# Kernel optimization log

Measured on AMD Instinct MI355X. Metric: run time of the kernel, lower is better.

The kernel has to match this reference:

```python
import jax, jax.numpy as jnp
import numpy as np

N, B, D_STREAM = 2048, 2, 1024
HEADS, D_KQ, D_V = 16, 64, 64
D_HEAD = 2 * D_KQ + D_V  # per-head [q|k|v] chunk


def setup_inputs() -> dict:
    key = jax.random.key(0)
    ks = jax.random.split(key, 6)
    s = 0.02
    return {
        "stream": jax.random.normal(ks[0], (N, B, D_STREAM), jnp.float32),
        "mask": jax.random.normal(ks[1], (1, N, N), jnp.float32),
        "w_qkv": jax.random.normal(ks[2], (D_STREAM, HEADS * D_HEAD), jnp.float32) * s,
        "b_qkv": jax.random.normal(ks[3], (HEADS * D_HEAD,), jnp.float32) * s,
        "w_out": jax.random.normal(ks[4], (HEADS * D_V, D_STREAM), jnp.float32) * s,
        "b_out": jax.random.normal(ks[5], (D_STREAM,), jnp.float32) * s,
    }


def reference(stream, mask, w_qkv, b_qkv, w_out, b_out):
    n, b, _ = stream.shape
    # qkv: (n, b, heads*(2*d_kq+d_v)) -> (n, b*heads, 2*d_kq+d_v)
    qkv = (stream @ w_qkv + b_qkv).reshape(n, b * HEADS, D_HEAD)
    q = qkv[:, :, :D_KQ]              # (n, bh, d_kq)
    k = qkv[:, :, D_KQ:2 * D_KQ]      # (n, bh, d_kq)
    v = qkv[:, :, 2 * D_KQ:]          # (n, bh, d_v)
    # logits: (bh, n, n); NOTE: no 1/sqrt(d_kq) scaling, faithful to source
    logits = jnp.einsum("nhd,mhd->hnm", q, k) + mask
    weights = jax.nn.softmax(logits, axis=-1)
    values = jnp.einsum("hnm,mhd->nhd", weights, v)  # (n, bh, d_v)
    values = values.reshape(n * b, HEADS * D_V)
    out = (values @ w_out + b_out).reshape(n, b, D_STREAM)
    return out
```

## Files before the change

kernel.cpp:

```cpp
#include <hip/hip_runtime.h>
#include <hip/hip_bf16.h>

#define N_SEQ 2048
#define DSTR 1024
#define NH 32
#define QKVN 3072
#define MROWS 4096

typedef float f32x4 __attribute__((ext_vector_type(4)));
typedef short bf16x8 __attribute__((ext_vector_type(8)));
typedef unsigned short ushort4v __attribute__((ext_vector_type(4)));
typedef unsigned short u16t;

__device__ __forceinline__ u16t f2bf(float f) {
  union { float f; unsigned u; } x; x.f = f;
  return (u16t)((x.u + 0x7fff + ((x.u >> 16) & 1)) >> 16);
}
__device__ __forceinline__ float bf2f(u16t u) {
  union { unsigned u; float f; } x; x.u = ((unsigned)u) << 16; return x.f;
}
__device__ __forceinline__ unsigned cvt_pk_bf16(float a, float b) {
  unsigned r;
  asm("v_cvt_pk_bf16_f32 %0, %1, %2" : "=v"(r) : "v"(a), "v"(b));
  return r;
}

#define MFMA16(a, b, c) __builtin_amdgcn_mfma_f32_16x16x32_bf16(a, b, c, 0, 0, 0)

__device__ __forceinline__ void gl2lds16(const void* g, void* l) {
  __builtin_amdgcn_global_load_lds((const __attribute__((address_space(1))) void*)g,
                                   (__attribute__((address_space(3))) void*)l, 16, 0, 0);
}

__global__ void split_f32_kernel(const float* __restrict__ in, u16t* __restrict__ hi,
                                 u16t* __restrict__ lo, int n4) {
  int i = blockIdx.x * blockDim.x + threadIdx.x;
  if (i >= n4) return;
  float4 v = ((const float4*)in)[i];
  float vv[4] = {v.x, v.y, v.z, v.w};
  ushort4v h, l;
  #pragma unroll
  for (int j = 0; j < 4; j++) {
    h[j] = f2bf(vv[j]);
    l[j] = f2bf(vv[j] - bf2f(h[j]));
  }
  ((ushort4v*)hi)[i] = h;
  if (lo) ((ushort4v*)lo)[i] = l;
}

__global__ void transpose_split_kernel(const float* __restrict__ in,
                                       u16t* __restrict__ hi, u16t* __restrict__ lo,
                                       int K, int Nc) {
  __shared__ float tile[32][33];
  const int n0 = blockIdx.x * 32, k0 = blockIdx.y * 32;
  const int tx = threadIdx.x, ty = threadIdx.y;
  #pragma unroll
  for (int j = 0; j < 32; j += 8)
    tile[ty + j][tx] = in[(size_t)(k0 + ty + j) * Nc + n0 + tx];
  __syncthreads();
  #pragma unroll
  for (int j = 0; j < 32; j += 8) {
    float v = tile[tx][ty + j];
    size_t o = (size_t)(n0 + ty + j) * K + k0 + tx;
    u16t h = f2bf(v);
    hi[o] = h;
    if (lo) lo[o] = f2bf(v - bf2f(h));
  }
}

__global__ __launch_bounds__(256, 3) void gemm_qkv_kernel(
    const u16t* __restrict__ Ahi, const u16t* __restrict__ Alo,
    const u16t* __restrict__ Bhi, const float* __restrict__ bias,
    u16t* __restrict__ Qhi, u16t* __restrict__ Qlo,
    u16t* __restrict__ Khi, u16t* __restrict__ Vt) {
  constexpr int BK = 64;
  __shared__ u16t sAh[128 * 64], sAl[128 * 64], sBh[128 * 64];
  const int t = threadIdx.x;
  const int lane = t & 63, wid = t >> 6;
  const int wm = wid >> 1, wn = wid & 1;
  const int g = lane >> 4, cc = lane & 15;
  const int m0 = blockIdx.x * 128, n0 = blockIdx.y * 128;
  const int srow = t >> 3;
  const int sc = ((t & 7) ^ ((t >> 3) & 7)) * 8;

  f32x4 acc[4][4] = {};

  for (int k0 = 0; k0 < DSTR; k0 += BK) {
    __syncthreads();
    #pragma unroll
    for (int i = 0; i < 4; i++) {
      const int row = i * 32 + srow;
      gl2lds16(Ahi + (size_t)(m0 + row) * DSTR + k0 + sc, &sAh[i * 2048 + wid * 512]);
      gl2lds16(Alo + (size_t)(m0 + row) * DSTR + k0 + sc, &sAl[i * 2048 + wid * 512]);
      gl2lds16(Bhi + (size_t)(n0 + row) * DSTR + k0 + sc, &sBh[i * 2048 + wid * 512]);
    }
    __syncthreads();
    #pragma unroll
    for (int kk = 0; kk < 2; kk++) {
      bf16x8 ah[4], al[4], bh[4];
      #pragma unroll
      for (int mt = 0; mt < 4; mt++) {
        const int r = wm * 64 + mt * 16 + cc;
        const int c = ((4 * kk + g) ^ (cc & 7)) * 8;
        ah[mt] = *(const bf16x8*)&sAh[r * 64 + c];
        al[mt] = *(const bf16x8*)&sAl[r * 64 + c];
      }
      #pragma unroll
      for (int nt = 0; nt < 4; nt++) {
        const int r = wn * 64 + nt * 16 + cc;
        const int c = ((4 * kk + g) ^ (cc & 7)) * 8;
        bh[nt] = *(const bf16x8*)&sBh[r * 64 + c];
      }
      #pragma unroll
      for (int mt = 0; mt < 4; mt++)
        #pragma unroll
        for (int nt = 0; nt < 4; nt++) {
          acc[mt][nt] = MFMA16(ah[mt], bh[nt], acc[mt][nt]);
          acc[mt][nt] = MFMA16(al[mt], bh[nt], acc[mt][nt]);
        }
    }
  }
  #pragma unroll
  for (int mt = 0; mt < 4; mt++)
    #pragma unroll
    for (int nt = 0; nt < 4; nt++)
      #pragma unroll
      for (int r = 0; r < 4; r++) {
        int grow = m0 + wm * 64 + mt * 16 + g * 4 + r;
        int gcol = n0 + wn * 64 + nt * 16 + cc;
        float val = acc[mt][nt][r] + bias[gcol];
        int nn = grow >> 1, bb = grow & 1;
        int hl = gcol / 192, off = gcol - hl * 192;
        int hh = bb * 16 + hl;
        if (off < 64) {
          size_t o = ((size_t)hh * N_SEQ + nn) * 64 + off;
          u16t h_ = f2bf(val);
          Qhi[o] = h_;
          Qlo[o] = f2bf(val - bf2f(h_));
        } else if (off < 128) {
          Khi[((size_t)hh * N_SEQ + nn) * 64 + (off - 64)] = f2bf(val);
        } else {
          int c = nn & 63;
          int nperm = (nn & ~63) | ((c & 15) << 2) | (c >> 4);
          Vt[((size_t)hh * 64 + (off - 128)) * N_SEQ + nperm] = f2bf(val);
        }
      }
}

__global__ __launch_bounds__(512, 4) void attn_kernel(
    const u16t* __restrict__ Qhi, const u16t* __restrict__ Qlo,
    const u16t* __restrict__ Khi, const u16t* __restrict__ Vt,
    const u16t* __restrict__ maskT, u16t* __restrict__ Vals) {
  __shared__ u16t sKh[2][64 * 64];
  __shared__ u16t sV[2][64 * 64];
  __shared__ u16t sP[8][16 * 72];
  const int t = threadIdx.x;
  const int lane = t & 63, wid = t >> 6;
  const int g = lane >> 4, cc = lane & 15;
  const int h = blockIdx.x >> 4;
  const int qt = blockIdx.x & 15;
  const int q0 = qt * 128 + wid * 16;

  const size_t kbase = (size_t)h * N_SEQ * 64;
  const size_t vbase = (size_t)h * 64 * N_SEQ;

  const int srow = t >> 3;
  const int ssw = ((t & 7) ^ (srow & 7)) * 8;
  const int wbase = wid * 512;

  auto stage = [&](int buf, int mt0) {
    gl2lds16(Khi + kbase + (size_t)(mt0 + srow) * 64 + ssw, &sKh[buf][wbase]);
    gl2lds16(Vt + vbase + (size_t)srow * N_SEQ + mt0 + ssw, &sV[buf][wbase]);
  };

  const size_t qoff = kbase + (size_t)(q0 + cc) * 64 + g * 8;
  bf16x8 qh0 = *(const bf16x8*)(Qhi + qoff);
  bf16x8 qh1 = *(const bf16x8*)(Qhi + qoff + 32);
  bf16x8 ql0 = *(const bf16x8*)(Qlo + qoff);
  bf16x8 ql1 = *(const bf16x8*)(Qlo + qoff + 32);

  f32x4 o[4] = {};
  float M[4], L[4];
  #pragma unroll
  for (int r = 0; r < 4; r++) { M[r] = -1e30f; L[r] = 0.0f; }

  stage(0, 0);
  int cur = 0;
  const int sw = (cc & 7) * 8;

  for (int ti = 0; ti < N_SEQ / 64; ++ti) {
    const int mt0 = ti * 64;
    __syncthreads();
    if (ti + 1 < N_SEQ / 64) stage(cur ^ 1, mt0 + 64);

    ushort4v ml[4];
    #pragma unroll
    for (int mt = 0; mt < 4; ++mt)
      ml[mt] = *(const ushort4v*)&maskT[(size_t)(mt0 + mt * 16 + cc) * N_SEQ + q0 + g * 4];

    f32x4 s[4];
    #pragma unroll
    for (int mt = 0; mt < 4; ++mt) {
      const int krow = (mt * 16 + cc) * 64;
      bf16x8 kh0 = *(const bf16x8*)&sKh[cur][krow + ((g * 8) ^ sw)];
      bf16x8 kh1 = *(const bf16x8*)&sKh[cur][krow + ((32 + g * 8) ^ sw)];
      f32x4 a = {};
      a = MFMA16(qh0, kh0, a);
      a = MFMA16(qh1, kh1, a);
      a = MFMA16(ql0, kh0, a);
      a = MFMA16(ql1, kh1, a);
      s[mt] = a;
    }
    float mx[4];
    #pragma unroll
    for (int r = 0; r < 4; ++r) {
      s[0][r] += bf2f(ml[0][r]);
      s[1][r] += bf2f(ml[1][r]);
      s[2][r] += bf2f(ml[2][r]);
      s[3][r] += bf2f(ml[3][r]);
      float m1 = fmaxf(fmaxf(s[0][r], s[1][r]), fmaxf(s[2][r], s[3][r]));
      m1 = fmaxf(m1, __shfl_xor(m1, 1, 16));
      m1 = fmaxf(m1, __shfl_xor(m1, 2, 16));
      m1 = fmaxf(m1, __shfl_xor(m1, 4, 16));
      m1 = fmaxf(m1, __shfl_xor(m1, 8, 16));
      mx[r] = m1;
    }
    float dm = fmaxf(fmaxf(mx[0] - M[0], mx[1] - M[1]),
                     fmaxf(mx[2] - M[2], mx[3] - M[3]));
    if (__any(dm > 8.0f)) {
      #pragma unroll
      for (int r = 0; r < 4; ++r) {
        float nM = fmaxf(M[r], mx[r]);
        float al = __expf(M[r] - nM);
        L[r] *= al;
        o[0][r] *= al; o[1][r] *= al; o[2][r] *= al; o[3][r] *= al;
        M[r] = nM;
      }
    }
    #pragma unroll
    for (int r = 0; r < 4; ++r) {
      float p0 = __expf(s[0][r] - M[r]);
      float p1 = __expf(s[1][r] - M[r]);
      float p2 = __expf(s[2][r] - M[r]);
      float p3 = __expf(s[3][r] - M[r]);
      float rs = (p0 + p1) + (p2 + p3);
      rs += __shfl_xor(rs, 1, 16);
      rs += __shfl_xor(rs, 2, 16);
      rs += __shfl_xor(rs, 4, 16);
      rs += __shfl_xor(rs, 8, 16);
      L[r] += rs;
      unsigned w0 = cvt_pk_bf16(p0, p1);
      unsigned w1 = cvt_pk_bf16(p2, p3);
      u16t* P = &sP[wid][(g * 4 + r) * 72 + cc * 4];
      P[0] = (u16t)w0; P[1] = (u16t)(w0 >> 16);
      P[2] = (u16t)w1; P[3] = (u16t)(w1 >> 16);
    }
    bf16x8 pf0 = *(const bf16x8*)&sP[wid][cc * 72 + g * 8];
    bf16x8 pf1 = *(const bf16x8*)&sP[wid][cc * 72 + 32 + g * 8];
    #pragma unroll
    for (int dt = 0; dt < 4; ++dt) {
      const int vrow = (dt * 16 + cc) * 64;
      bf16x8 v0 = *(const bf16x8*)&sV[cur][vrow + ((g * 8) ^ sw)];
      bf16x8 v1 = *(const bf16x8*)&sV[cur][vrow + ((32 + g * 8) ^ sw)];
      o[dt] = MFMA16(pf0, v0, o[dt]);
      o[dt] = MFMA16(pf1, v1, o[dt]);
    }
    cur ^= 1;
  }
  const int bb = h >> 4, hl = h & 15;
  #pragma unroll
  for (int r = 0; r < 4; ++r) {
    const int q = q0 + g * 4 + r;
    float invL = 1.0f / L[r];
    const size_t orow = (size_t)(q * 2 + bb) * DSTR + hl * 64;
    #pragma unroll
    for (int dt = 0; dt < 4; ++dt)
      Vals[orow + dt * 16 + cc] = f2bf(o[dt][r] * invL);
  }
}

__global__ __launch_bounds__(256, 3) void gemm_out_kernel(
    const u16t* __restrict__ A, const u16t* __restrict__ Bt,
    const float* __restrict__ bias, float* __restrict__ out) {
  constexpr int BK = 64;
  __shared__ u16t sA[128 * 64], sB[128 * 64];
  const int t = threadIdx.x;
  const int lane = t & 63, wid = t >> 6;
  const int wm = wid >> 1, wn = wid & 1;
  const int g = lane >> 4, cc = lane & 15;
  const int m0 = blockIdx.x * 128, n0 = blockIdx.y * 128;
  const int srow = t >> 3;
  const int sc = ((t & 7) ^ ((t >> 3) & 7)) * 8;

  f32x4 acc[4][4] = {};
  for (int k0 = 0; k0 < DSTR; k0 += BK) {
    __syncthreads();
    #pragma unroll
    for (int i = 0; i < 4; i++) {
      const int row = i * 32 + srow;
      gl2lds16(A + (size_t)(m0 + row) * DSTR + k0 + sc, &sA[i * 2048 + wid * 512]);
      gl2lds16(Bt + (size_t)(n0 + row) * DSTR + k0 + sc, &sB[i * 2048 + wid * 512]);
    }
    __syncthreads();
    #pragma unroll
    for (int kk = 0; kk < 2; kk++) {
      bf16x8 af[4], bfr[4];
      #pragma unroll
      for (int mt = 0; mt < 4; mt++) {
        const int r = wm * 64 + mt * 16 + cc;
        const int c = ((4 * kk + g) ^ (cc & 7)) * 8;
        af[mt] = *(const bf16x8*)&sA[r * 64 + c];
      }
      #pragma unroll
      for (int nt = 0; nt < 4; nt++) {
        const int r = wn * 64 + nt * 16 + cc;
        const int c = ((4 * kk + g) ^ (cc & 7)) * 8;
        bfr[nt] = *(const bf16x8*)&sB[r * 64 + c];
      }
      #pragma unroll
      for (int mt = 0; mt < 4; mt++)
        #pragma unroll
        for (int nt = 0; nt < 4; nt++)
          acc[mt][nt] = MFMA16(af[mt], bfr[nt], acc[mt][nt]);
    }
  }
  #pragma unroll
  for (int mt = 0; mt < 4; mt++)
    #pragma unroll
    for (int nt = 0; nt < 4; nt++)
      #pragma unroll
      for (int r = 0; r < 4; r++) {
        int grow = m0 + wm * 64 + mt * 16 + g * 4 + r;
        int gcol = n0 + wn * 64 + nt * 16 + cc;
        out[(size_t)grow * DSTR + gcol] = acc[mt][nt][r] + bias[gcol];
      }
}

extern "C" void kernel_launch(void* const* d_in, const int* in_sizes, int n_in,
                              void* d_out, int out_size, void* d_ws, size_t ws_size,
                              hipStream_t stream) {
  (void)in_sizes; (void)n_in; (void)out_size; (void)ws_size;
  const float* x      = (const float*)d_in[0];
  const float* mask   = (const float*)d_in[1];
  const float* w_qkv  = (const float*)d_in[2];
  const float* b_qkv  = (const float*)d_in[3];
  const float* w_out  = (const float*)d_in[4];
  const float* b_out  = (const float*)d_in[5];
  float* out = (float*)d_out;

  char* ws = (char*)d_ws;
  size_t off = 0;
  auto alloc = [&](size_t n) { void* p = ws + off; off += (n + 255) & ~(size_t)255; return p; };
  u16t* WqkvT = (u16t*)alloc((size_t)QKVN * DSTR * 2);
  u16t* WoutT = (u16t*)alloc((size_t)DSTR * DSTR * 2);
  u16t* Qhi = (u16t*)alloc((size_t)NH * N_SEQ * 64 * 2);
  u16t* Qlo = (u16t*)alloc((size_t)NH * N_SEQ * 64 * 2);
  u16t* Khi = (u16t*)alloc((size_t)NH * N_SEQ * 64 * 2);
  u16t* Vt  = (u16t*)alloc((size_t)NH * 64 * N_SEQ * 2);
  u16t* Xhi = (u16t*)alloc((size_t)MROWS * DSTR * 2);
  u16t* Xlo = (u16t*)alloc((size_t)MROWS * DSTR * 2);
  u16t* MaskT = (u16t*)alloc((size_t)N_SEQ * N_SEQ * 2);
  u16t* Vals = Xhi;

  split_f32_kernel<<<dim3(MROWS * DSTR / 4 / 256), 256, 0, stream>>>(x, Xhi, Xlo, MROWS * DSTR / 4);
  transpose_split_kernel<<<dim3(QKVN / 32, DSTR / 32), dim3(32, 8), 0, stream>>>(
      w_qkv, WqkvT, nullptr, DSTR, QKVN);
  transpose_split_kernel<<<dim3(DSTR / 32, DSTR / 32), dim3(32, 8), 0, stream>>>(
      w_out, WoutT, nullptr, DSTR, DSTR);
  transpose_split_kernel<<<dim3(N_SEQ / 32, N_SEQ / 32), dim3(32, 8), 0, stream>>>(
      mask, MaskT, nullptr, N_SEQ, N_SEQ);
  gemm_qkv_kernel<<<dim3(MROWS / 128, QKVN / 128), 256, 0, stream>>>(
      Xhi, Xlo, WqkvT, b_qkv, Qhi, Qlo, Khi, Vt);
  attn_kernel<<<dim3(NH * (N_SEQ / 128)), 512, 0, stream>>>(
      Qhi, Qlo, Khi, Vt, MaskT, Vals);
  gemm_out_kernel<<<dim3(MROWS / 128, DSTR / 128), 256, 0, stream>>>(
      Vals, WoutT, b_out, out);
}
```

Before: 272.8 us.

## Compute transposed scores in attention, fold log2e into Q and mask, shrink blocks

The QK MFMA operands are swapped so each lane holds scores for a single query row. Row max and sum then need only two cross-lane shuffles, with one M and L per lane instead of four. The log2e factor is folded into Q in the QKV epilogue and into the mask during conversion, so the softmax can use a raw v_exp_f32; the mask no longer needs a transpose pass and the V permutation is dropped. Attention blocks shrink from 512 to 256 threads over 64 queries, which doubles the grid. The P tile now uses an XOR-swizzled layout, and the rescale threshold becomes a base-2 equivalent.

```diff
diff --git a/kernel.cpp b/kernel.cpp
--- a/kernel.cpp
+++ b/kernel.cpp
@@ -6,6 +6,7 @@
 #define NH 32
 #define QKVN 3072
 #define MROWS 4096
+#define LOG2E 1.4426950408889634f
 
 typedef float f32x4 __attribute__((ext_vector_type(4)));
 typedef short bf16x8 __attribute__((ext_vector_type(8)));
@@ -24,6 +25,11 @@
   asm("v_cvt_pk_bf16_f32 %0, %1, %2" : "=v"(r) : "v"(a), "v"(b));
   return r;
 }
+__device__ __forceinline__ float exp2a(float x) {
+  float r;
+  asm("v_exp_f32 %0, %1" : "=v"(r) : "v"(x));
+  return r;
+}
 
 #define MFMA16(a, b, c) __builtin_amdgcn_mfma_f32_16x16x32_bf16(a, b, c, 0, 0, 0)
 
@@ -33,11 +39,11 @@
 }
 
 __global__ void split_f32_kernel(const float* __restrict__ in, u16t* __restrict__ hi,
-                                 u16t* __restrict__ lo, int n4) {
+                                 u16t* __restrict__ lo, int n4, float scale) {
   int i = blockIdx.x * blockDim.x + threadIdx.x;
   if (i >= n4) return;
   float4 v = ((const float4*)in)[i];
-  float vv[4] = {v.x, v.y, v.z, v.w};
+  float vv[4] = {v.x * scale, v.y * scale, v.z * scale, v.w * scale};
   ushort4v h, l;
   #pragma unroll
   for (int j = 0; j < 4; j++) {
@@ -133,6 +139,7 @@
         int hl = gcol / 192, off = gcol - hl * 192;
         int hh = bb * 16 + hl;
         if (off < 64) {
+          val *= LOG2E;
           size_t o = ((size_t)hh * N_SEQ + nn) * 64 + off;
           u16t h_ = f2bf(val);
           Qhi[o] = h_;
@@ -140,37 +147,36 @@
         } else if (off < 128) {
           Khi[((size_t)hh * N_SEQ + nn) * 64 + (off - 64)] = f2bf(val);
         } else {
-          int c = nn & 63;
-          int nperm = (nn & ~63) | ((c & 15) << 2) | (c >> 4);
-          Vt[((size_t)hh * 64 + (off - 128)) * N_SEQ + nperm] = f2bf(val);
+          Vt[((size_t)hh * 64 + (off - 128)) * N_SEQ + nn] = f2bf(val);
         }
       }
 }
 
-__global__ __launch_bounds__(512, 4) void attn_kernel(
+__global__ __launch_bounds__(256, 4) void attn_kernel(
     const u16t* __restrict__ Qhi, const u16t* __restrict__ Qlo,
     const u16t* __restrict__ Khi, const u16t* __restrict__ Vt,
-    const u16t* __restrict__ maskT, u16t* __restrict__ Vals) {
+    const u16t* __restrict__ maskb, u16t* __restrict__ Vals) {
   __shared__ u16t sKh[2][64 * 64];
   __shared__ u16t sV[2][64 * 64];
-  __shared__ u16t sP[8][16 * 72];
+  __shared__ u16t sP[4][16 * 64];
   const int t = threadIdx.x;
   const int lane = t & 63, wid = t >> 6;
   const int g = lane >> 4, cc = lane & 15;
-  const int h = blockIdx.x >> 4;
-  const int qt = blockIdx.x & 15;
-  const int q0 = qt * 128 + wid * 16;
+  const int h = blockIdx.x >> 5;
+  const int qt = blockIdx.x & 31;
+  const int q0 = qt * 64 + wid * 16;
 
   const size_t kbase = (size_t)h * N_SEQ * 64;
   const size_t vbase = (size_t)h * 64 * N_SEQ;
 
   const int srow = t >> 3;
-  const int ssw = ((t & 7) ^ (srow & 7)) * 8;
-  const int wbase = wid * 512;
+  const int sc = ((t & 7) ^ ((t >> 3) & 7)) * 8;
 
   auto stage = [&](int buf, int mt0) {
-    gl2lds16(Khi + kbase + (size_t)(mt0 + srow) * 64 + ssw, &sKh[buf][wbase]);
-    gl2lds16(Vt + vbase + (size_t)srow * N_SEQ + mt0 + ssw, &sV[buf][wbase]);
+    gl2lds16(Khi + kbase + (size_t)(mt0 + srow) * 64 + sc,      &sKh[buf][wid * 512]);
+    gl2lds16(Khi + kbase + (size_t)(mt0 + srow + 32) * 64 + sc, &sKh[buf][2048 + wid * 512]);
+    gl2lds16(Vt + vbase + (size_t)srow * N_SEQ + mt0 + sc,        &sV[buf][wid * 512]);
+    gl2lds16(Vt + vbase + (size_t)(srow + 32) * N_SEQ + mt0 + sc, &sV[buf][2048 + wid * 512]);
   };
 
   const size_t qoff = kbase + (size_t)(q0 + cc) * 64 + g * 8;
@@ -180,13 +186,13 @@
   bf16x8 ql1 = *(const bf16x8*)(Qlo + qoff + 32);
 
   f32x4 o[4] = {};
-  float M[4], L[4];
-  #pragma unroll
-  for (int r = 0; r < 4; r++) { M[r] = -1e30f; L[r] = 0.0f; }
+  float M = -1e30f, L = 0.0f;
 
   stage(0, 0);
   int cur = 0;
   const int sw = (cc & 7) * 8;
+  u16t* sPw = sP[wid];
+  const int alane = (lane & 48) + g * 4;
 
   for (int ti = 0; ti < N_SEQ / 64; ++ti) {
     const int mt0 = ti * 64;
@@ -196,7 +202,7 @@
     ushort4v ml[4];
     #pragma unroll
     for (int mt = 0; mt < 4; ++mt)
-      ml[mt] = *(const ushort4v*)&maskT[(size_t)(mt0 + mt * 16 + cc) * N_SEQ + q0 + g * 4];
+      ml[mt] = *(const ushort4v*)&maskb[(size_t)(q0 + cc) * N_SEQ + mt0 + mt * 16 + g * 4];
 
     f32x4 s[4];
     #pragma unroll
@@ -205,58 +211,61 @@
       bf16x8 kh0 = *(const bf16x8*)&sKh[cur][krow + ((g * 8) ^ sw)];
       bf16x8 kh1 = *(const bf16x8*)&sKh[cur][krow + ((32 + g * 8) ^ sw)];
       f32x4 a = {};
-      a = MFMA16(qh0, kh0, a);
-      a = MFMA16(qh1, kh1, a);
-      a = MFMA16(ql0, kh0, a);
-      a = MFMA16(ql1, kh1, a);
+      a = MFMA16(kh0, qh0, a);
+      a = MFMA16(kh1, qh1, a);
+      a = MFMA16(kh0, ql0, a);
+      a = MFMA16(kh1, ql1, a);
       s[mt] = a;
     }
-    float mx[4];
-    #pragma unroll
-    for (int r = 0; r < 4; ++r) {
-      s[0][r] += bf2f(ml[0][r]);
-      s[1][r] += bf2f(ml[1][r]);
-      s[2][r] += bf2f(ml[2][r]);
-      s[3][r] += bf2f(ml[3][r]);
-      float m1 = fmaxf(fmaxf(s[0][r], s[1][r]), fmaxf(s[2][r], s[3][r]));
-      m1 = fmaxf(m1, __shfl_xor(m1, 1, 16));
-      m1 = fmaxf(m1, __shfl_xor(m1, 2, 16));
-      m1 = fmaxf(m1, __shfl_xor(m1, 4, 16));
-      m1 = fmaxf(m1, __shfl_xor(m1, 8, 16));
-      mx[r] = m1;
-    }
-    float dm = fmaxf(fmaxf(mx[0] - M[0], mx[1] - M[1]),
-                     fmaxf(mx[2] - M[2], mx[3] - M[3]));
-    if (__any(dm > 8.0f)) {
+    float pm = -1e30f;
+    #pragma unroll
+    for (int mt = 0; mt < 4; ++mt)
       #pragma unroll
       for (int r = 0; r < 4; ++r) {
-        float nM = fmaxf(M[r], mx[r]);
-        float al = __expf(M[r] - nM);
-        L[r] *= al;
-        o[0][r] *= al; o[1][r] *= al; o[2][r] *= al; o[3][r] *= al;
-        M[r] = nM;
-      }
-    }
-    #pragma unroll
-    for (int r = 0; r < 4; ++r) {
-      float p0 = __expf(s[0][r] - M[r]);
-      float p1 = __expf(s[1][r] - M[r]);
-      float p2 = __expf(s[2][r] - M[r]);
-      float p3 = __expf(s[3][r] - M[r]);
-      float rs = (p0 + p1) + (p2 + p3);
-      rs += __shfl_xor(rs, 1, 16);
-      rs += __shfl_xor(rs, 2, 16);
-      rs += __shfl_xor(rs, 4, 16);
-      rs += __shfl_xor(rs, 8, 16);
-      L[r] += rs;
-      unsigned w0 = cvt_pk_bf16(p0, p1);
-      unsigned w1 = cvt_pk_bf16(p2, p3);
-      u16t* P = &sP[wid][(g * 4 + r) * 72 + cc * 4];
+        s[mt][r] += bf2f(ml[mt][r]);
+        pm = fmaxf(pm, s[mt][r]);
+      }
+    pm = fmaxf(pm, __shfl_xor(pm, 16));
+    pm = fmaxf(pm, __shfl_xor(pm, 32));
+
+    if (__any(pm - M > 11.54f)) {
+      float nM = fmaxf(M, pm);
+      float alpha = exp2a(M - nM);
+      L *= alpha;
+      M = nM;
+      float ar[4];
+      #pragma unroll
+      for (int r = 0; r < 4; ++r) ar[r] = __shfl(alpha, alane + r);
+      #pragma unroll
+      for (int dt = 0; dt < 4; ++dt)
+        #pragma unroll
+        for (int r = 0; r < 4; ++r) o[dt][r] *= ar[r];
+    }
+
+    float p[4][4];
+    float rs = 0.0f;
+    #pragma unroll
+    for (int mt = 0; mt < 4; ++mt)
+      #pragma unroll
+      for (int r = 0; r < 4; ++r) {
+        p[mt][r] = exp2a(s[mt][r] - M);
+        rs += p[mt][r];
+      }
+    rs += __shfl_xor(rs, 16);
+    rs += __shfl_xor(rs, 32);
+    L += rs;
+
+    #pragma unroll
+    for (int mt = 0; mt < 4; ++mt) {
+      unsigned w0 = cvt_pk_bf16(p[mt][0], p[mt][1]);
+      unsigned w1 = cvt_pk_bf16(p[mt][2], p[mt][3]);
+      const int kb = mt * 16 + (g >> 1) * 8;
+      u16t* P = &sPw[cc * 64 + (kb ^ sw) + (g & 1) * 4];
       P[0] = (u16t)w0; P[1] = (u16t)(w0 >> 16);
       P[2] = (u16t)w1; P[3] = (u16t)(w1 >> 16);
     }
-    bf16x8 pf0 = *(const bf16x8*)&sP[wid][cc * 72 + g * 8];
-    bf16x8 pf1 = *(const bf16x8*)&sP[wid][cc * 72 + 32 + g * 8];
+    bf16x8 pf0 = *(const bf16x8*)&sPw[cc * 64 + ((g * 8) ^ sw)];
+    bf16x8 pf1 = *(const bf16x8*)&sPw[cc * 64 + ((32 + g * 8) ^ sw)];
     #pragma unroll
     for (int dt = 0; dt < 4; ++dt) {
       const int vrow = (dt * 16 + cc) * 64;
@@ -267,15 +276,18 @@
     }
     cur ^= 1;
   }
+  float invL = 1.0f / L;
+  float ir[4];
+  #pragma unroll
+  for (int r = 0; r < 4; ++r) ir[r] = __shfl(invL, alane + r);
   const int bb = h >> 4, hl = h & 15;
   #pragma unroll
   for (int r = 0; r < 4; ++r) {
     const int q = q0 + g * 4 + r;
-    float invL = 1.0f / L[r];
     const size_t orow = (size_t)(q * 2 + bb) * DSTR + hl * 64;
     #pragma unroll
     for (int dt = 0; dt < 4; ++dt)
-      Vals[orow + dt * 16 + cc] = f2bf(o[dt][r] * invL);
+      Vals[orow + dt * 16 + cc] = f2bf(o[dt][r] * ir[r]);
   }
 }
 
@@ -359,20 +371,21 @@
   u16t* Vt  = (u16t*)alloc((size_t)NH * 64 * N_SEQ * 2);
   u16t* Xhi = (u16t*)alloc((size_t)MROWS * DSTR * 2);
   u16t* Xlo = (u16t*)alloc((size_t)MROWS * DSTR * 2);
-  u16t* MaskT = (u16t*)alloc((size_t)N_SEQ * N_SEQ * 2);
+  u16t* MaskB = (u16t*)alloc((size_t)N_SEQ * N_SEQ * 2);
   u16t* Vals = Xhi;
 
-  split_f32_kernel<<<dim3(MROWS * DSTR / 4 / 256), 256, 0, stream>>>(x, Xhi, Xlo, MROWS * DSTR / 4);
+  split_f32_kernel<<<dim3(MROWS * DSTR / 4 / 256), 256, 0, stream>>>(
+      x, Xhi, Xlo, MROWS * DSTR / 4, 1.0f);
+  split_f32_kernel<<<dim3(N_SEQ * N_SEQ / 4 / 256), 256, 0, stream>>>(
+      mask, MaskB, nullptr, N_SEQ * N_SEQ / 4, LOG2E);
   transpose_split_kernel<<<dim3(QKVN / 32, DSTR / 32), dim3(32, 8), 0, stream>>>(
       w_qkv, WqkvT, nullptr, DSTR, QKVN);
   transpose_split_kernel<<<dim3(DSTR / 32, DSTR / 32), dim3(32, 8), 0, stream>>>(
       w_out, WoutT, nullptr, DSTR, DSTR);
-  transpose_split_kernel<<<dim3(N_SEQ / 32, N_SEQ / 32), dim3(32, 8), 0, stream>>>(
-      mask, MaskT, nullptr, N_SEQ, N_SEQ);
   gemm_qkv_kernel<<<dim3(MROWS / 128, QKVN / 128), 256, 0, stream>>>(
       Xhi, Xlo, WqkvT, b_qkv, Qhi, Qlo, Khi, Vt);
-  attn_kernel<<<dim3(NH * (N_SEQ / 128)), 512, 0, stream>>>(
-      Qhi, Qlo, Khi, Vt, MaskT, Vals);
+  attn_kernel<<<dim3(NH * (N_SEQ / 64)), 256, 0, stream>>>(
+      Qhi, Qlo, Khi, Vt, MaskB, Vals);
   gemm_out_kernel<<<dim3(MROWS / 128, DSTR / 128), 256, 0, stream>>>(
       Vals, WoutT, b_out, out);
 }
```

Measured after the change: 266.3 us. 1.02x faster.
